# Optimization experiments

Hardware: AMD Instinct MI355X
Metric: run time of the kernel (lower is better)

Reference implementation:

```python
import jax, jax.numpy as jnp
import numpy as np

NUM_CODES = 512
CODE_DIM = 64
COMMITMENT_COST = 0.1
DECAY = 0.9
EPS = 1e-5


def setup_inputs() -> dict:
    key = jax.random.key(0)
    k1, k2, k3 = jax.random.split(key, 3)
    B, L, D, K = 32, 4096, CODE_DIM, NUM_CODES
    z_e = jax.random.normal(k1, (B, L, D), dtype=jnp.float32)
    emb = jax.random.uniform(k2, (K, D), dtype=jnp.float32, minval=-1.0 / K, maxval=1.0 / K)
    ema_cluster_size = jnp.ones((K,), dtype=jnp.float32)
    ema_w = emb + 0.01 * jax.random.normal(k3, (K, D), dtype=jnp.float32)
    return {"z_e": z_e, "emb": emb, "ema_cluster_size": ema_cluster_size, "ema_w": ema_w}


def reference(z_e, emb, ema_cluster_size, ema_w):
    B, L, D = z_e.shape
    K = emb.shape[0]
    flat = z_e.reshape(-1, D)                                   # [N, D]
    dists = (jnp.sum(flat * flat, axis=1, keepdims=True)
             - 2.0 * flat @ emb.T
             + jnp.sum(emb * emb, axis=1)[None, :])
    codes = jnp.argmin(dists, axis=1)                           # [N] int
    z_q = emb[codes].reshape(B, L, D)
    # straight-through estimator
    z_q_st = z_e + jax.lax.stop_gradient(z_q - z_e)
    # EMA updates (training, no_grad) via direct scatter-reduce instead of one-hot matmul
    cluster_size = jax.ops.segment_sum(jnp.ones_like(codes, dtype=z_e.dtype), codes, num_segments=K)
    new_ecs = ema_cluster_size * DECAY + cluster_size * (1.0 - DECAY)
    dw = jax.ops.segment_sum(flat, codes, num_segments=K)       # [K, D]
    new_ema_w = ema_w * DECAY + dw * (1.0 - DECAY)
    n = jnp.sum(new_ecs)
    cs_smoothed = (new_ecs + EPS) / (n + K * EPS) * n
    new_emb = new_ema_w / (cs_smoothed[:, None] + EPS)
    # commitment loss (z_q detached)
    commit = jnp.mean((z_e - jax.lax.stop_gradient(z_q)) ** 2)
    loss_vq = COMMITMENT_COST * commit
    return (z_q_st, loss_vq, codes.reshape(B, L), new_ecs, new_ema_w, new_emb)
```

## Files before the change

### kernel.cpp

```cpp
#include <hip/hip_runtime.h>
#include <math.h>

#define NROWS 131072
#define DIM 64
#define NCODE 512
#define FLAG_CAP 32768
#define THR 6e-5f

#define OUT_ZQ    0
#define OUT_LOSS  8388608
#define OUT_CODES 8388609
#define OUT_ECS   8519681
#define OUT_EMAW  8520193
#define OUT_EMB   8552961

#define WS_LOSS    0
#define WS_N       8
#define WS_FLAGC   12
#define WS_COUNTS  16
#define WS_OFFSETS 2064
#define WS_CURSOR  4112
#define WS_CSUM    6160
#define WS_EHI     8208
#define WS_ELO     73744
#define WS_CODESI  139280
#define WS_DW4     139280
#define WS_BUCKET  663568
#define WS_FLAGR   663568
#define WS_BYTES   1187856
#define WS_ZERO_BYTES 2064

#define DECAY_C ((float)0.9)
#define OMD_C   ((float)(1.0 - 0.9))
#define EPS_C   ((float)1e-5)

typedef float f32x4 __attribute__((ext_vector_type(4)));
typedef short short8v __attribute__((ext_vector_type(8)));

__device__ __forceinline__ unsigned short bf16_rne_bits(float f) {
    unsigned int u = __float_as_uint(f);
    unsigned int r = u + 0x7fffu + ((u >> 16) & 1u);
    return (unsigned short)(r >> 16);
}

__device__ __forceinline__ float np_pairwise64_sq(const float* v) {
    float r[8];
#pragma unroll
    for (int j = 0; j < 8; ++j) r[j] = __fmul_rn(v[j], v[j]);
#pragma unroll
    for (int b = 1; b < 8; ++b) {
#pragma unroll
        for (int j = 0; j < 8; ++j)
            r[j] = __fadd_rn(r[j], __fmul_rn(v[8 * b + j], v[8 * b + j]));
    }
    return __fadd_rn(__fadd_rn(__fadd_rn(r[0], r[1]), __fadd_rn(r[2], r[3])),
                     __fadd_rn(__fadd_rn(r[4], r[5]), __fadd_rn(r[6], r[7])));
}

__global__ void k_csum(const float* __restrict__ emb, float* __restrict__ csum) {
    int k = blockIdx.x * blockDim.x + threadIdx.x;
    if (k >= NCODE) return;
    float e[DIM];
#pragma unroll
    for (int d = 0; d < DIM; d += 4) {
        float4 v = *reinterpret_cast<const float4*>(emb + (size_t)k * DIM + d);
        e[d] = v.x; e[d + 1] = v.y; e[d + 2] = v.z; e[d + 3] = v.w;
    }
    csum[k] = np_pairwise64_sq(e);
}

__global__ __launch_bounds__(256) void k_split(
        const float* __restrict__ emb, unsigned short* __restrict__ ehi,
        unsigned short* __restrict__ elo) {
    int i = blockIdx.x * 256 + threadIdx.x;
    if (i >= NCODE * DIM) return;
    float v = emb[i];
    unsigned short h = bf16_rne_bits(v);
    float hf = __uint_as_float((unsigned int)h << 16);
    ehi[i] = h;
    elo[i] = bf16_rne_bits(v - hf);
}

#define CVTE(H, L, j, val) { \
    unsigned int ub = __float_as_uint(val); \
    unsigned int rr = ub + 0x7fffu + ((ub >> 16) & 1u); \
    unsigned short hb = (unsigned short)(rr >> 16); \
    float hf2 = __uint_as_float(((unsigned int)hb) << 16); \
    float lof = (val) - hf2; \
    unsigned int ul = __float_as_uint(lof); \
    unsigned int rl = ul + 0x7fffu + ((ul >> 16) & 1u); \
    H[j] = (short)hb; L[j] = (short)(rl >> 16); }

__global__ __launch_bounds__(256, 1) void k_mfma(
        const float* __restrict__ ze, const unsigned short* __restrict__ ehi,
        const unsigned short* __restrict__ elo, const float* __restrict__ csum,
        float* __restrict__ out, int* __restrict__ codes_i,
        int* __restrict__ flagC, int* __restrict__ flagR) {
    __shared__ float cs[NCODE];
    for (int i = threadIdx.x; i < NCODE; i += 256) cs[i] = csum[i];
    __syncthreads();
    int wid = threadIdx.x >> 6;
    int lane = threadIdx.x & 63;
    int r16 = lane & 15;
    int kg = lane >> 4;
    int rowbase = blockIdx.x * 128 + wid * 32;

    short8v ahi[2][2], alo[2][2];
#define LOADA(rt, hf) { \
        const float4* ap = reinterpret_cast<const float4*>( \
            ze + (size_t)(rowbase + (rt) * 16 + r16) * DIM + (hf) * 32 + 8 * kg); \
        float4 u = ap[0], w = ap[1]; \
        CVTE(ahi[rt][hf], alo[rt][hf], 0, u.x) CVTE(ahi[rt][hf], alo[rt][hf], 1, u.y) \
        CVTE(ahi[rt][hf], alo[rt][hf], 2, u.z) CVTE(ahi[rt][hf], alo[rt][hf], 3, u.w) \
        CVTE(ahi[rt][hf], alo[rt][hf], 4, w.x) CVTE(ahi[rt][hf], alo[rt][hf], 5, w.y) \
        CVTE(ahi[rt][hf], alo[rt][hf], 6, w.z) CVTE(ahi[rt][hf], alo[rt][hf], 7, w.w) }
    LOADA(0, 0) LOADA(0, 1) LOADA(1, 0) LOADA(1, 1)

    float m1v[2][4], m2v[2][4];
    int i1v[2][4];
#pragma unroll
    for (int rt = 0; rt < 2; ++rt)
#pragma unroll
        for (int j = 0; j < 4; ++j) { m1v[rt][j] = 3.4e38f; m2v[rt][j] = 3.4e38f; i1v[rt][j] = 0; }

#define UPD(C, rt, reg) { \
        float s = __builtin_fmaf(-2.f, C[reg], csv); \
        if (s < m1v[rt][reg]) { m2v[rt][reg] = m1v[rt][reg]; m1v[rt][reg] = s; i1v[rt][reg] = codeIdx; } \
        else if (s < m2v[rt][reg]) { m2v[rt][reg] = s; } }

    for (int t = 0; t < 32; ++t) {
        const short8v* bh = reinterpret_cast<const short8v*>(
            ehi + (size_t)(t * 16 + r16) * DIM + 8 * kg);
        const short8v* bl = reinterpret_cast<const short8v*>(
            elo + (size_t)(t * 16 + r16) * DIM + 8 * kg);
        short8v bh0 = bh[0], bh1 = bh[4];
        short8v bl0 = bl[0], bl1 = bl[4];
        f32x4 c0 = {0.f, 0.f, 0.f, 0.f};
        f32x4 c1 = {0.f, 0.f, 0.f, 0.f};
        c0 = __builtin_amdgcn_mfma_f32_16x16x32_bf16(ahi[0][0], bh0, c0, 0, 0, 0);
        c0 = __builtin_amdgcn_mfma_f32_16x16x32_bf16(ahi[0][1], bh1, c0, 0, 0, 0);
        c0 = __builtin_amdgcn_mfma_f32_16x16x32_bf16(alo[0][0], bh0, c0, 0, 0, 0);
        c0 = __builtin_amdgcn_mfma_f32_16x16x32_bf16(alo[0][1], bh1, c0, 0, 0, 0);
        c0 = __builtin_amdgcn_mfma_f32_16x16x32_bf16(ahi[0][0], bl0, c0, 0, 0, 0);
        c0 = __builtin_amdgcn_mfma_f32_16x16x32_bf16(ahi[0][1], bl1, c0, 0, 0, 0);
        c1 = __builtin_amdgcn_mfma_f32_16x16x32_bf16(ahi[1][0], bh0, c1, 0, 0, 0);
        c1 = __builtin_amdgcn_mfma_f32_16x16x32_bf16(ahi[1][1], bh1, c1, 0, 0, 0);
        c1 = __builtin_amdgcn_mfma_f32_16x16x32_bf16(alo[1][0], bh0, c1, 0, 0, 0);
        c1 = __builtin_amdgcn_mfma_f32_16x16x32_bf16(alo[1][1], bh1, c1, 0, 0, 0);
        c1 = __builtin_amdgcn_mfma_f32_16x16x32_bf16(ahi[1][0], bl0, c1, 0, 0, 0);
        c1 = __builtin_amdgcn_mfma_f32_16x16x32_bf16(ahi[1][1], bl1, c1, 0, 0, 0);
        float csv = cs[t * 16 + r16];
        int codeIdx = t * 16 + r16;
        UPD(c0, 0, 0) UPD(c0, 0, 1) UPD(c0, 0, 2) UPD(c0, 0, 3)
        UPD(c1, 1, 0) UPD(c1, 1, 1) UPD(c1, 1, 2) UPD(c1, 1, 3)
    }

#define RED(rt, reg, mask) { \
        float om1 = __shfl_xor(m1v[rt][reg], mask); \
        int   oi  = __shfl_xor(i1v[rt][reg], mask); \
        float om2 = __shfl_xor(m2v[rt][reg], mask); \
        if (om1 < m1v[rt][reg]) { \
            m2v[rt][reg] = fminf(m1v[rt][reg], om2); m1v[rt][reg] = om1; i1v[rt][reg] = oi; \
        } else if (om1 > m1v[rt][reg]) { \
            m2v[rt][reg] = fminf(m2v[rt][reg], om1); \
        } else { \
            if (oi < i1v[rt][reg]) i1v[rt][reg] = oi; \
            m2v[rt][reg] = m1v[rt][reg]; } }
#define RED4(rt, reg) RED(rt, reg, 1) RED(rt, reg, 2) RED(rt, reg, 4) RED(rt, reg, 8)
    RED4(0, 0) RED4(0, 1) RED4(0, 2) RED4(0, 3)
    RED4(1, 0) RED4(1, 1) RED4(1, 2) RED4(1, 3)

    if (r16 == 0) {
        int g = lane >> 4;
#define WOUT(rt, reg) { \
        int row = rowbase + (rt) * 16 + 4 * g + (reg); \
        out[OUT_CODES + row] = (float)i1v[rt][reg]; \
        codes_i[row] = i1v[rt][reg]; \
        if (m2v[rt][reg] - m1v[rt][reg] < THR) { \
            int pos = atomicAdd(flagC, 1); \
            if (pos < FLAG_CAP) flagR[pos] = row; } }
        WOUT(0, 0) WOUT(0, 1) WOUT(0, 2) WOUT(0, 3)
        WOUT(1, 0) WOUT(1, 1) WOUT(1, 2) WOUT(1, 3)
    }
}

__global__ __launch_bounds__(64) void k_rescue(
        const float* __restrict__ ze, const float* __restrict__ emb,
        const float* __restrict__ csum, float* __restrict__ out,
        int* __restrict__ codes_i, const int* __restrict__ flagC,
        const int* __restrict__ flagR) {
    __shared__ float x2s[DIM];
    int nf = *flagC;
    if (nf > FLAG_CAP) nf = FLAG_CAP;
    int lane = threadIdx.x;
    for (int i = blockIdx.x; i < nf; i += gridDim.x) {
        int row = flagR[i];
        __syncthreads();
        float v = ze[(size_t)row * DIM + lane];
        x2s[lane] = __fadd_rn(v, v);
        __syncthreads();
        float r[8];
#pragma unroll
        for (int j = 0; j < 8; ++j) r[j] = __fmul_rn(x2s[j], x2s[j]);
#pragma unroll
        for (int b = 1; b < 8; ++b) {
#pragma unroll
            for (int j = 0; j < 8; ++j)
                r[j] = __fadd_rn(r[j], __fmul_rn(x2s[8 * b + j], x2s[8 * b + j]));
        }
        float A = __fmul_rn(0.25f,
            __fadd_rn(__fadd_rn(__fadd_rn(r[0], r[1]), __fadd_rn(r[2], r[3])),
                      __fadd_rn(__fadd_rn(r[4], r[5]), __fadd_rn(r[6], r[7]))));
        float m1 = 3.4e38f;
        int i1 = 0x7fffffff;
#pragma unroll
        for (int kk = 0; kk < 8; ++kk) {
            int k = lane * 8 + kk;
            const float* e = emb + (size_t)k * DIM;
            float a = 0.f;
#pragma unroll
            for (int d = 0; d < DIM; ++d) a = __builtin_fmaf(x2s[d], e[d], a);
            float t = __fadd_rn(__fsub_rn(A, a), csum[k]);
            if (t < m1) { m1 = t; i1 = k; }
        }
        for (int off = 32; off; off >>= 1) {
            float ov = __shfl_xor(m1, off);
            int oi = __shfl_xor(i1, off);
            if (ov < m1 || (ov == m1 && oi < i1)) { m1 = ov; i1 = oi; }
        }
        if (lane == 0) {
            out[OUT_CODES + row] = (float)i1;
            codes_i[row] = i1;
        }
    }
}

__global__ __launch_bounds__(256) void k_apply(
        const float* __restrict__ ze, const float* __restrict__ emb,
        const int* __restrict__ codes_i, float* __restrict__ out,
        int* __restrict__ counts, double* __restrict__ lossAcc) {
    __shared__ int h[NCODE];
    __shared__ double ls[4];
    int t = threadIdx.x;
    for (int i = t; i < NCODE; i += 256) h[i] = 0;
    __syncthreads();
    int row = blockIdx.x * 256 + t;
    int code = codes_i[row];
    atomicAdd(&h[code], 1);
    const float* x = ze + (size_t)row * DIM;
    const float* e = emb + (size_t)code * DIM;
    float* zq = out + OUT_ZQ + (size_t)row * DIM;
    double lsum = 0.0;
#pragma unroll
    for (int d = 0; d < DIM; d += 4) {
        float4 xv = *reinterpret_cast<const float4*>(x + d);
        float4 ev = *reinterpret_cast<const float4*>(e + d);
        float ta = __fsub_rn(ev.x, xv.x);
        float tb = __fsub_rn(ev.y, xv.y);
        float tc = __fsub_rn(ev.z, xv.z);
        float td = __fsub_rn(ev.w, xv.w);
        float4 o;
        o.x = __fadd_rn(xv.x, ta);
        o.y = __fadd_rn(xv.y, tb);
        o.z = __fadd_rn(xv.z, tc);
        o.w = __fadd_rn(xv.w, td);
        *reinterpret_cast<float4*>(zq + d) = o;
        lsum += (double)ta * ta + (double)tb * tb + (double)tc * tc + (double)td * td;
    }
    for (int off = 32; off; off >>= 1) lsum += __shfl_down(lsum, off);
    int wid = t >> 6;
    if ((t & 63) == 0) ls[wid] = lsum;
    __syncthreads();
    if (t == 0) atomicAdd(lossAcc, (ls[0] + ls[1]) + (ls[2] + ls[3]));
    for (int k = t; k < NCODE; k += 256) {
        int cc = h[k];
        if (cc) atomicAdd(&counts[k], cc);
    }
}

__global__ __launch_bounds__(512) void k_scan(
        const int* __restrict__ counts, int* __restrict__ offsets, int* __restrict__ cursor,
        const float* __restrict__ ecs_in, float* __restrict__ out, float* __restrict__ n_out) {
    __shared__ int sa[NCODE], sb[NCODE];
    __shared__ float red[NCODE];
    int k = threadIdx.x;
    int c = counts[k];
    sa[k] = c;
    float v = __fadd_rn(__fmul_rn(ecs_in[k], DECAY_C), __fmul_rn((float)c, OMD_C));
    out[OUT_ECS + k] = v;
    red[k] = v;
    __syncthreads();
    int* src = sa;
    int* dst = sb;
    for (int off = 1; off < NCODE; off <<= 1) {
        dst[k] = (k >= off) ? src[k - off] + src[k] : src[k];
        __syncthreads();
        int* tp = src; src = dst; dst = tp;
    }
    offsets[k] = src[k] - c;
    cursor[k]  = src[k] - c;
    for (int s = NCODE / 2; s > 0; s >>= 1) {
        if (k < s) red[k] += red[k + s];
        __syncthreads();
    }
    if (k == 0) n_out[0] = red[0];
}

__global__ __launch_bounds__(256) void k_scatter(
        const int* __restrict__ codes_i, int* __restrict__ cursor, int* __restrict__ bucket) {
    int row = blockIdx.x * 256 + threadIdx.x;
    int c = codes_i[row];
    int pos = atomicAdd(&cursor[c], 1);
    bucket[pos] = row;
}

__global__ __launch_bounds__(256) void k_dw(
        const float* __restrict__ ze, const int* __restrict__ bucket,
        const int* __restrict__ offsets, const int* __restrict__ counts,
        float* __restrict__ dw4) {
    __shared__ float p[4][DIM];
    int k = blockIdx.x >> 2;
    int q = blockIdx.x & 3;
    int w = threadIdx.x >> 6;
    int d = threadIdx.x & 63;
    int s = offsets[k];
    int n = counts[k];
    float acc0 = 0.f, acc1 = 0.f;
    int i = q + 4 * w;
    for (; i + 16 < n; i += 32) {
        int ra = bucket[s + i];
        int rb = bucket[s + i + 16];
        acc0 += ze[(size_t)ra * DIM + d];
        acc1 += ze[(size_t)rb * DIM + d];
    }
    if (i < n) acc0 += ze[(size_t)bucket[s + i] * DIM + d];
    p[w][d] = acc0 + acc1;
    __syncthreads();
    if (w == 0) dw4[((size_t)q * NCODE + k) * DIM + d] = (p[0][d] + p[1][d]) + (p[2][d] + p[3][d]);
}

__global__ __launch_bounds__(256) void k_final(
        const float* __restrict__ ema_w, const float* __restrict__ dw4,
        const float* __restrict__ n_ptr, const double* __restrict__ lossAcc,
        float* __restrict__ out) {
    int i = blockIdx.x * blockDim.x + threadIdx.x;
    if (i >= NCODE * DIM) return;
    int k = i >> 6;
    float dsum = __fadd_rn(__fadd_rn(dw4[i], dw4[i + NCODE * DIM]),
                           __fadd_rn(dw4[i + 2 * NCODE * DIM], dw4[i + 3 * NCODE * DIM]));
    float w = __fadd_rn(__fmul_rn(ema_w[i], DECAY_C), __fmul_rn(dsum, OMD_C));
    out[OUT_EMAW + i] = w;
    float n = n_ptr[0];
    float necs = out[OUT_ECS + k];
    float cs = (necs + EPS_C) / (n + (float)NCODE * EPS_C) * n;
    out[OUT_EMB + i] = w / (cs + EPS_C);
    if (i == 0) out[OUT_LOSS] = (float)(0.1 * (lossAcc[0] / (double)((size_t)NROWS * DIM)));
}

extern "C" void kernel_launch(void* const* d_in, const int* in_sizes, int n_in,
                              void* d_out, int out_size, void* d_ws, size_t ws_size,
                              hipStream_t stream) {
    const float* ze   = (const float*)d_in[0];
    const float* emb  = (const float*)d_in[1];
    const float* ecs  = (const float*)d_in[2];
    const float* emaw = (const float*)d_in[3];
    float* out = (float*)d_out;
    char* ws = (char*)d_ws;
    double* lossAcc = (double*)(ws + WS_LOSS);
    float*  n_out   = (float*)(ws + WS_N);
    int*    flagC   = (int*)(ws + WS_FLAGC);
    int*    counts  = (int*)(ws + WS_COUNTS);
    int*    offsets = (int*)(ws + WS_OFFSETS);
    int*    cursor  = (int*)(ws + WS_CURSOR);
    float*  csum    = (float*)(ws + WS_CSUM);
    unsigned short* ehi = (unsigned short*)(ws + WS_EHI);
    unsigned short* elo = (unsigned short*)(ws + WS_ELO);
    int*    codes_i = (int*)(ws + WS_CODESI);
    float*  dw4     = (float*)(ws + WS_DW4);
    int*    bucket  = (int*)(ws + WS_BUCKET);
    int*    flagR   = (int*)(ws + WS_FLAGR);

    hipMemsetAsync(d_ws, 0, WS_ZERO_BYTES, stream);
    hipLaunchKernelGGL(k_csum, dim3(2), dim3(256), 0, stream, emb, csum);
    hipLaunchKernelGGL(k_split, dim3(NCODE * DIM / 256), dim3(256), 0, stream, emb, ehi, elo);
    hipLaunchKernelGGL(k_mfma, dim3(NROWS / 128), dim3(256), 0, stream,
                       ze, ehi, elo, csum, out, codes_i, flagC, flagR);
    hipLaunchKernelGGL(k_rescue, dim3(1024), dim3(64), 0, stream,
                       ze, emb, csum, out, codes_i, flagC, flagR);
    hipLaunchKernelGGL(k_apply, dim3(NROWS / 256), dim3(256), 0, stream,
                       ze, emb, codes_i, out, counts, lossAcc);
    hipLaunchKernelGGL(k_scan, dim3(1), dim3(512), 0, stream,
                       counts, offsets, cursor, ecs, out, n_out);
    hipLaunchKernelGGL(k_scatter, dim3(NROWS / 256), dim3(256), 0, stream,
                       codes_i, cursor, bucket);
    hipLaunchKernelGGL(k_dw, dim3(NCODE * 4), dim3(256), 0, stream,
                       ze, bucket, offsets, counts, dw4);
    hipLaunchKernelGGL(k_final, dim3(NCODE * DIM / 256), dim3(256), 0, stream,
                       emaw, dw4, n_out, lossAcc, out);
}
```

Before: 225.9 us.

## Fuse z_q gather, loss and histogram into MFMA kernel; patch rescued rows incrementally

The separate apply kernel is removed. The MFMA argmin kernel now writes z_q, accumulates the commitment loss and builds the per-code histogram itself, so z_e is not reread in an extra pass and one launch goes away. The rescue kernel only touches rows whose code actually changes, fixing counts, z_q and the loss by delta. Each block now covers 64 rows instead of 128 (one 16-row tile per wave), and the occupancy hint in launch_bounds is dropped. The cost is less reuse of the B tiles per wave, and the double-precision loss sum is now accumulated in a different order.

```diff
diff --git a/kernel.cpp b/kernel.cpp
--- a/kernel.cpp
+++ b/kernel.cpp
@@ -91,42 +91,45 @@
     unsigned int rl = ul + 0x7fffu + ((ul >> 16) & 1u); \
     H[j] = (short)hb; L[j] = (short)(rl >> 16); }
 
-__global__ __launch_bounds__(256, 1) void k_mfma(
-        const float* __restrict__ ze, const unsigned short* __restrict__ ehi,
-        const unsigned short* __restrict__ elo, const float* __restrict__ csum,
-        float* __restrict__ out, int* __restrict__ codes_i,
-        int* __restrict__ flagC, int* __restrict__ flagR) {
+__global__ __launch_bounds__(256) void k_mfma(
+        const float* __restrict__ ze, const float* __restrict__ emb,
+        const unsigned short* __restrict__ ehi, const unsigned short* __restrict__ elo,
+        const float* __restrict__ csum, float* __restrict__ out,
+        int* __restrict__ codes_i, int* __restrict__ counts,
+        double* __restrict__ lossAcc, int* __restrict__ flagC, int* __restrict__ flagR) {
     __shared__ float cs[NCODE];
-    for (int i = threadIdx.x; i < NCODE; i += 256) cs[i] = csum[i];
-    __syncthreads();
-    int wid = threadIdx.x >> 6;
-    int lane = threadIdx.x & 63;
+    __shared__ int h[NCODE];
+    __shared__ int code_s[64];
+    __shared__ double ls[4];
+    int tid = threadIdx.x;
+    for (int i = tid; i < NCODE; i += 256) { cs[i] = csum[i]; h[i] = 0; }
+    __syncthreads();
+    int wid = tid >> 6;
+    int lane = tid & 63;
     int r16 = lane & 15;
     int kg = lane >> 4;
-    int rowbase = blockIdx.x * 128 + wid * 32;
-
-    short8v ahi[2][2], alo[2][2];
-#define LOADA(rt, hf) { \
+    int blockRow = blockIdx.x * 64;
+    int waveRow = blockRow + wid * 16;
+
+    short8v ahi[2], alo[2];
+#define LOADA(hf) { \
         const float4* ap = reinterpret_cast<const float4*>( \
-            ze + (size_t)(rowbase + (rt) * 16 + r16) * DIM + (hf) * 32 + 8 * kg); \
+            ze + (size_t)(waveRow + r16) * DIM + (hf) * 32 + 8 * kg); \
         float4 u = ap[0], w = ap[1]; \
-        CVTE(ahi[rt][hf], alo[rt][hf], 0, u.x) CVTE(ahi[rt][hf], alo[rt][hf], 1, u.y) \
-        CVTE(ahi[rt][hf], alo[rt][hf], 2, u.z) CVTE(ahi[rt][hf], alo[rt][hf], 3, u.w) \
-        CVTE(ahi[rt][hf], alo[rt][hf], 4, w.x) CVTE(ahi[rt][hf], alo[rt][hf], 5, w.y) \
-        CVTE(ahi[rt][hf], alo[rt][hf], 6, w.z) CVTE(ahi[rt][hf], alo[rt][hf], 7, w.w) }
-    LOADA(0, 0) LOADA(0, 1) LOADA(1, 0) LOADA(1, 1)
-
-    float m1v[2][4], m2v[2][4];
-    int i1v[2][4];
-#pragma unroll
-    for (int rt = 0; rt < 2; ++rt)
-#pragma unroll
-        for (int j = 0; j < 4; ++j) { m1v[rt][j] = 3.4e38f; m2v[rt][j] = 3.4e38f; i1v[rt][j] = 0; }
-
-#define UPD(C, rt, reg) { \
-        float s = __builtin_fmaf(-2.f, C[reg], csv); \
-        if (s < m1v[rt][reg]) { m2v[rt][reg] = m1v[rt][reg]; m1v[rt][reg] = s; i1v[rt][reg] = codeIdx; } \
-        else if (s < m2v[rt][reg]) { m2v[rt][reg] = s; } }
+        CVTE(ahi[hf], alo[hf], 0, u.x) CVTE(ahi[hf], alo[hf], 1, u.y) \
+        CVTE(ahi[hf], alo[hf], 2, u.z) CVTE(ahi[hf], alo[hf], 3, u.w) \
+        CVTE(ahi[hf], alo[hf], 4, w.x) CVTE(ahi[hf], alo[hf], 5, w.y) \
+        CVTE(ahi[hf], alo[hf], 6, w.z) CVTE(ahi[hf], alo[hf], 7, w.w) }
+    LOADA(0) LOADA(1)
+
+    float m1v[4] = {3.4e38f, 3.4e38f, 3.4e38f, 3.4e38f};
+    float m2v[4] = {3.4e38f, 3.4e38f, 3.4e38f, 3.4e38f};
+    int i1v[4] = {0, 0, 0, 0};
+
+#define UPD(reg) { \
+        float s = __builtin_fmaf(-2.f, c[reg], csv); \
+        if (s < m1v[reg]) { m2v[reg] = m1v[reg]; m1v[reg] = s; i1v[reg] = codeIdx; } \
+        else if (s < m2v[reg]) { m2v[reg] = s; } }
 
     for (int t = 0; t < 32; ++t) {
         const short8v* bh = reinterpret_cast<const short8v*>(
@@ -135,59 +138,73 @@
             elo + (size_t)(t * 16 + r16) * DIM + 8 * kg);
         short8v bh0 = bh[0], bh1 = bh[4];
         short8v bl0 = bl[0], bl1 = bl[4];
-        f32x4 c0 = {0.f, 0.f, 0.f, 0.f};
-        f32x4 c1 = {0.f, 0.f, 0.f, 0.f};
-        c0 = __builtin_amdgcn_mfma_f32_16x16x32_bf16(ahi[0][0], bh0, c0, 0, 0, 0);
-        c0 = __builtin_amdgcn_mfma_f32_16x16x32_bf16(ahi[0][1], bh1, c0, 0, 0, 0);
-        c0 = __builtin_amdgcn_mfma_f32_16x16x32_bf16(alo[0][0], bh0, c0, 0, 0, 0);
-        c0 = __builtin_amdgcn_mfma_f32_16x16x32_bf16(alo[0][1], bh1, c0, 0, 0, 0);
-        c0 = __builtin_amdgcn_mfma_f32_16x16x32_bf16(ahi[0][0], bl0, c0, 0, 0, 0);
-        c0 = __builtin_amdgcn_mfma_f32_16x16x32_bf16(ahi[0][1], bl1, c0, 0, 0, 0);
-        c1 = __builtin_amdgcn_mfma_f32_16x16x32_bf16(ahi[1][0], bh0, c1, 0, 0, 0);
-        c1 = __builtin_amdgcn_mfma_f32_16x16x32_bf16(ahi[1][1], bh1, c1, 0, 0, 0);
-        c1 = __builtin_amdgcn_mfma_f32_16x16x32_bf16(alo[1][0], bh0, c1, 0, 0, 0);
-        c1 = __builtin_amdgcn_mfma_f32_16x16x32_bf16(alo[1][1], bh1, c1, 0, 0, 0);
-        c1 = __builtin_amdgcn_mfma_f32_16x16x32_bf16(ahi[1][0], bl0, c1, 0, 0, 0);
-        c1 = __builtin_amdgcn_mfma_f32_16x16x32_bf16(ahi[1][1], bl1, c1, 0, 0, 0);
+        f32x4 c = {0.f, 0.f, 0.f, 0.f};
+        c = __builtin_amdgcn_mfma_f32_16x16x32_bf16(ahi[0], bh0, c, 0, 0, 0);
+        c = __builtin_amdgcn_mfma_f32_16x16x32_bf16(ahi[1], bh1, c, 0, 0, 0);
+        c = __builtin_amdgcn_mfma_f32_16x16x32_bf16(alo[0], bh0, c, 0, 0, 0);
+        c = __builtin_amdgcn_mfma_f32_16x16x32_bf16(alo[1], bh1, c, 0, 0, 0);
+        c = __builtin_amdgcn_mfma_f32_16x16x32_bf16(ahi[0], bl0, c, 0, 0, 0);
+        c = __builtin_amdgcn_mfma_f32_16x16x32_bf16(ahi[1], bl1, c, 0, 0, 0);
         float csv = cs[t * 16 + r16];
         int codeIdx = t * 16 + r16;
-        UPD(c0, 0, 0) UPD(c0, 0, 1) UPD(c0, 0, 2) UPD(c0, 0, 3)
-        UPD(c1, 1, 0) UPD(c1, 1, 1) UPD(c1, 1, 2) UPD(c1, 1, 3)
-    }
-
-#define RED(rt, reg, mask) { \
-        float om1 = __shfl_xor(m1v[rt][reg], mask); \
-        int   oi  = __shfl_xor(i1v[rt][reg], mask); \
-        float om2 = __shfl_xor(m2v[rt][reg], mask); \
-        if (om1 < m1v[rt][reg]) { \
-            m2v[rt][reg] = fminf(m1v[rt][reg], om2); m1v[rt][reg] = om1; i1v[rt][reg] = oi; \
-        } else if (om1 > m1v[rt][reg]) { \
-            m2v[rt][reg] = fminf(m2v[rt][reg], om1); \
+        UPD(0) UPD(1) UPD(2) UPD(3)
+    }
+
+#define RED(reg, mask) { \
+        float om1 = __shfl_xor(m1v[reg], mask); \
+        int   oi  = __shfl_xor(i1v[reg], mask); \
+        float om2 = __shfl_xor(m2v[reg], mask); \
+        if (om1 < m1v[reg]) { \
+            m2v[reg] = fminf(m1v[reg], om2); m1v[reg] = om1; i1v[reg] = oi; \
+        } else if (om1 > m1v[reg]) { \
+            m2v[reg] = fminf(m2v[reg], om1); \
         } else { \
-            if (oi < i1v[rt][reg]) i1v[rt][reg] = oi; \
-            m2v[rt][reg] = m1v[rt][reg]; } }
-#define RED4(rt, reg) RED(rt, reg, 1) RED(rt, reg, 2) RED(rt, reg, 4) RED(rt, reg, 8)
-    RED4(0, 0) RED4(0, 1) RED4(0, 2) RED4(0, 3)
-    RED4(1, 0) RED4(1, 1) RED4(1, 2) RED4(1, 3)
+            if (oi < i1v[reg]) i1v[reg] = oi; \
+            m2v[reg] = m1v[reg]; } }
+#define RED4(reg) RED(reg, 1) RED(reg, 2) RED(reg, 4) RED(reg, 8)
+    RED4(0) RED4(1) RED4(2) RED4(3)
 
     if (r16 == 0) {
-        int g = lane >> 4;
-#define WOUT(rt, reg) { \
-        int row = rowbase + (rt) * 16 + 4 * g + (reg); \
-        out[OUT_CODES + row] = (float)i1v[rt][reg]; \
-        codes_i[row] = i1v[rt][reg]; \
-        if (m2v[rt][reg] - m1v[rt][reg] < THR) { \
+#define WOUT(reg) { \
+        int lrow = wid * 16 + 4 * kg + (reg); \
+        int row = blockRow + lrow; \
+        code_s[lrow] = i1v[reg]; \
+        out[OUT_CODES + row] = (float)i1v[reg]; \
+        codes_i[row] = i1v[reg]; \
+        atomicAdd(&h[i1v[reg]], 1); \
+        if (m2v[reg] - m1v[reg] < THR) { \
             int pos = atomicAdd(flagC, 1); \
             if (pos < FLAG_CAP) flagR[pos] = row; } }
-        WOUT(0, 0) WOUT(0, 1) WOUT(0, 2) WOUT(0, 3)
-        WOUT(1, 0) WOUT(1, 1) WOUT(1, 2) WOUT(1, 3)
+        WOUT(0) WOUT(1) WOUT(2) WOUT(3)
+    }
+    __syncthreads();
+
+    double lpart = 0.0;
+#pragma unroll 4
+    for (int r = 0; r < 16; ++r) {
+        int code = code_s[wid * 16 + r];
+        int row = waveRow + r;
+        float x = ze[(size_t)row * DIM + lane];
+        float e = emb[(size_t)code * DIM + lane];
+        float tdiff = __fsub_rn(e, x);
+        out[OUT_ZQ + (size_t)row * DIM + lane] = __fadd_rn(x, tdiff);
+        lpart += (double)tdiff * tdiff;
+    }
+    for (int off = 32; off; off >>= 1) lpart += __shfl_down(lpart, off);
+    if (lane == 0) ls[wid] = lpart;
+    __syncthreads();
+    if (tid == 0) atomicAdd(lossAcc, (ls[0] + ls[1]) + (ls[2] + ls[3]));
+    for (int k = tid; k < NCODE; k += 256) {
+        int cc = h[k];
+        if (cc) atomicAdd(&counts[k], cc);
     }
 }
 
 __global__ __launch_bounds__(64) void k_rescue(
         const float* __restrict__ ze, const float* __restrict__ emb,
         const float* __restrict__ csum, float* __restrict__ out,
-        int* __restrict__ codes_i, const int* __restrict__ flagC,
+        int* __restrict__ codes_i, int* __restrict__ counts,
+        double* __restrict__ lossAcc, const int* __restrict__ flagC,
         const int* __restrict__ flagR) {
     __shared__ float x2s[DIM];
     int nf = *flagC;
@@ -228,53 +245,24 @@
             int oi = __shfl_xor(i1, off);
             if (ov < m1 || (ov == m1 && oi < i1)) { m1 = ov; i1 = oi; }
         }
-        if (lane == 0) {
-            out[OUT_CODES + row] = (float)i1;
-            codes_i[row] = i1;
+        int oldc = codes_i[row];
+        if (i1 != oldc) {
+            if (lane == 0) {
+                codes_i[row] = i1;
+                out[OUT_CODES + row] = (float)i1;
+                atomicSub(&counts[oldc], 1);
+                atomicAdd(&counts[i1], 1);
+            }
+            float x = __fmul_rn(0.5f, x2s[lane]);
+            float en = emb[(size_t)i1 * DIM + lane];
+            float eo = emb[(size_t)oldc * DIM + lane];
+            float tn = __fsub_rn(en, x);
+            float to = __fsub_rn(eo, x);
+            out[OUT_ZQ + (size_t)row * DIM + lane] = __fadd_rn(x, tn);
+            double dl = (double)tn * tn - (double)to * to;
+            for (int off = 32; off; off >>= 1) dl += __shfl_down(dl, off);
+            if (lane == 0) atomicAdd(lossAcc, dl);
         }
-    }
-}
-
-__global__ __launch_bounds__(256) void k_apply(
-        const float* __restrict__ ze, const float* __restrict__ emb,
-        const int* __restrict__ codes_i, float* __restrict__ out,
-        int* __restrict__ counts, double* __restrict__ lossAcc) {
-    __shared__ int h[NCODE];
-    __shared__ double ls[4];
-    int t = threadIdx.x;
-    for (int i = t; i < NCODE; i += 256) h[i] = 0;
-    __syncthreads();
-    int row = blockIdx.x * 256 + t;
-    int code = codes_i[row];
-    atomicAdd(&h[code], 1);
-    const float* x = ze + (size_t)row * DIM;
-    const float* e = emb + (size_t)code * DIM;
-    float* zq = out + OUT_ZQ + (size_t)row * DIM;
-    double lsum = 0.0;
-#pragma unroll
-    for (int d = 0; d < DIM; d += 4) {
-        float4 xv = *reinterpret_cast<const float4*>(x + d);
-        float4 ev = *reinterpret_cast<const float4*>(e + d);
-        float ta = __fsub_rn(ev.x, xv.x);
-        float tb = __fsub_rn(ev.y, xv.y);
-        float tc = __fsub_rn(ev.z, xv.z);
-        float td = __fsub_rn(ev.w, xv.w);
-        float4 o;
-        o.x = __fadd_rn(xv.x, ta);
-        o.y = __fadd_rn(xv.y, tb);
-        o.z = __fadd_rn(xv.z, tc);
-        o.w = __fadd_rn(xv.w, td);
-        *reinterpret_cast<float4*>(zq + d) = o;
-        lsum += (double)ta * ta + (double)tb * tb + (double)tc * tc + (double)td * td;
-    }
-    for (int off = 32; off; off >>= 1) lsum += __shfl_down(lsum, off);
-    int wid = t >> 6;
-    if ((t & 63) == 0) ls[wid] = lsum;
-    __syncthreads();
-    if (t == 0) atomicAdd(lossAcc, (ls[0] + ls[1]) + (ls[2] + ls[3]));
-    for (int k = t; k < NCODE; k += 256) {
-        int cc = h[k];
-        if (cc) atomicAdd(&counts[k], cc);
     }
 }
 
@@ -383,12 +371,10 @@
     hipMemsetAsync(d_ws, 0, WS_ZERO_BYTES, stream);
     hipLaunchKernelGGL(k_csum, dim3(2), dim3(256), 0, stream, emb, csum);
     hipLaunchKernelGGL(k_split, dim3(NCODE * DIM / 256), dim3(256), 0, stream, emb, ehi, elo);
-    hipLaunchKernelGGL(k_mfma, dim3(NROWS / 128), dim3(256), 0, stream,
-                       ze, ehi, elo, csum, out, codes_i, flagC, flagR);
+    hipLaunchKernelGGL(k_mfma, dim3(NROWS / 64), dim3(256), 0, stream,
+                       ze, emb, ehi, elo, csum, out, codes_i, counts, lossAcc, flagC, flagR);
     hipLaunchKernelGGL(k_rescue, dim3(1024), dim3(64), 0, stream,
-                       ze, emb, csum, out, codes_i, flagC, flagR);
-    hipLaunchKernelGGL(k_apply, dim3(NROWS / 256), dim3(256), 0, stream,
-                       ze, emb, codes_i, out, counts, lossAcc);
+                       ze, emb, csum, out, codes_i, counts, lossAcc, flagC, flagR);
     hipLaunchKernelGGL(k_scan, dim3(1), dim3(512), 0, stream,
                        counts, offsets, cursor, ecs, out, n_out);
     hipLaunchKernelGGL(k_scatter, dim3(NROWS / 256), dim3(256), 0, stream,
```

Result: slower. 310.5 us (+37.5%).

## Fuse z_q gather, loss, and code histogram into the MFMA argmin kernel

Applied to the files above, without the earlier changes.

Removes the separate apply kernel by computing the code histogram, the z_q straight-through output and the commitment loss inside the MFMA kernel, right after the argmin. The rescue kernel now applies corrections as deltas: it adjusts counts, rewrites z_q and adds the loss difference when a flagged row's code changes. This saves a full extra read of z_e and a kernel launch. In exchange the MFMA kernel carries more work, and the rescue path gains atomics.

```diff
diff --git a/kernel.cpp b/kernel.cpp
--- a/kernel.cpp
+++ b/kernel.cpp
@@ -92,15 +92,20 @@
     H[j] = (short)hb; L[j] = (short)(rl >> 16); }
 
 __global__ __launch_bounds__(256, 1) void k_mfma(
-        const float* __restrict__ ze, const unsigned short* __restrict__ ehi,
-        const unsigned short* __restrict__ elo, const float* __restrict__ csum,
-        float* __restrict__ out, int* __restrict__ codes_i,
-        int* __restrict__ flagC, int* __restrict__ flagR) {
+        const float* __restrict__ ze, const float* __restrict__ emb,
+        const unsigned short* __restrict__ ehi, const unsigned short* __restrict__ elo,
+        const float* __restrict__ csum, float* __restrict__ out,
+        int* __restrict__ codes_i, int* __restrict__ counts,
+        double* __restrict__ lossAcc, int* __restrict__ flagC, int* __restrict__ flagR) {
     __shared__ float cs[NCODE];
-    for (int i = threadIdx.x; i < NCODE; i += 256) cs[i] = csum[i];
-    __syncthreads();
-    int wid = threadIdx.x >> 6;
-    int lane = threadIdx.x & 63;
+    __shared__ int h[NCODE];
+    __shared__ int code_s[128];
+    __shared__ double ls[4];
+    int tid = threadIdx.x;
+    for (int i = tid; i < NCODE; i += 256) { cs[i] = csum[i]; h[i] = 0; }
+    __syncthreads();
+    int wid = tid >> 6;
+    int lane = tid & 63;
     int r16 = lane & 15;
     int kg = lane >> 4;
     int rowbase = blockIdx.x * 128 + wid * 32;
@@ -171,23 +176,47 @@
     RED4(1, 0) RED4(1, 1) RED4(1, 2) RED4(1, 3)
 
     if (r16 == 0) {
-        int g = lane >> 4;
 #define WOUT(rt, reg) { \
-        int row = rowbase + (rt) * 16 + 4 * g + (reg); \
+        int lrow = wid * 32 + (rt) * 16 + 4 * kg + (reg); \
+        int row = blockIdx.x * 128 + lrow; \
+        code_s[lrow] = i1v[rt][reg]; \
         out[OUT_CODES + row] = (float)i1v[rt][reg]; \
         codes_i[row] = i1v[rt][reg]; \
+        atomicAdd(&h[i1v[rt][reg]], 1); \
         if (m2v[rt][reg] - m1v[rt][reg] < THR) { \
             int pos = atomicAdd(flagC, 1); \
             if (pos < FLAG_CAP) flagR[pos] = row; } }
         WOUT(0, 0) WOUT(0, 1) WOUT(0, 2) WOUT(0, 3)
         WOUT(1, 0) WOUT(1, 1) WOUT(1, 2) WOUT(1, 3)
     }
+    __syncthreads();
+
+    double lpart = 0.0;
+#pragma unroll 4
+    for (int r = 0; r < 32; ++r) {
+        int code = code_s[wid * 32 + r];
+        int row = rowbase + r;
+        float x = ze[(size_t)row * DIM + lane];
+        float e = emb[(size_t)code * DIM + lane];
+        float tdiff = __fsub_rn(e, x);
+        out[OUT_ZQ + (size_t)row * DIM + lane] = __fadd_rn(x, tdiff);
+        lpart += (double)tdiff * tdiff;
+    }
+    for (int off = 32; off; off >>= 1) lpart += __shfl_down(lpart, off);
+    if (lane == 0) ls[wid] = lpart;
+    __syncthreads();
+    if (tid == 0) atomicAdd(lossAcc, (ls[0] + ls[1]) + (ls[2] + ls[3]));
+    for (int k = tid; k < NCODE; k += 256) {
+        int cc = h[k];
+        if (cc) atomicAdd(&counts[k], cc);
+    }
 }
 
 __global__ __launch_bounds__(64) void k_rescue(
         const float* __restrict__ ze, const float* __restrict__ emb,
         const float* __restrict__ csum, float* __restrict__ out,
-        int* __restrict__ codes_i, const int* __restrict__ flagC,
+        int* __restrict__ codes_i, int* __restrict__ counts,
+        double* __restrict__ lossAcc, const int* __restrict__ flagC,
         const int* __restrict__ flagR) {
     __shared__ float x2s[DIM];
     int nf = *flagC;
@@ -228,53 +257,24 @@
             int oi = __shfl_xor(i1, off);
             if (ov < m1 || (ov == m1 && oi < i1)) { m1 = ov; i1 = oi; }
         }
-        if (lane == 0) {
-            out[OUT_CODES + row] = (float)i1;
-            codes_i[row] = i1;
+        int oldc = codes_i[row];
+        if (i1 != oldc) {
+            if (lane == 0) {
+                codes_i[row] = i1;
+                out[OUT_CODES + row] = (float)i1;
+                atomicSub(&counts[oldc], 1);
+                atomicAdd(&counts[i1], 1);
+            }
+            float x = __fmul_rn(0.5f, x2s[lane]);
+            float en = emb[(size_t)i1 * DIM + lane];
+            float eo = emb[(size_t)oldc * DIM + lane];
+            float tn = __fsub_rn(en, x);
+            float to = __fsub_rn(eo, x);
+            out[OUT_ZQ + (size_t)row * DIM + lane] = __fadd_rn(x, tn);
+            double dl = (double)tn * tn - (double)to * to;
+            for (int off = 32; off; off >>= 1) dl += __shfl_down(dl, off);
+            if (lane == 0) atomicAdd(lossAcc, dl);
         }
-    }
-}
-
-__global__ __launch_bounds__(256) void k_apply(
-        const float* __restrict__ ze, const float* __restrict__ emb,
-        const int* __restrict__ codes_i, float* __restrict__ out,
-        int* __restrict__ counts, double* __restrict__ lossAcc) {
-    __shared__ int h[NCODE];
-    __shared__ double ls[4];
-    int t = threadIdx.x;
-    for (int i = t; i < NCODE; i += 256) h[i] = 0;
-    __syncthreads();
-    int row = blockIdx.x * 256 + t;
-    int code = codes_i[row];
-    atomicAdd(&h[code], 1);
-    const float* x = ze + (size_t)row * DIM;
-    const float* e = emb + (size_t)code * DIM;
-    float* zq = out + OUT_ZQ + (size_t)row * DIM;
-    double lsum = 0.0;
-#pragma unroll
-    for (int d = 0; d < DIM; d += 4) {
-        float4 xv = *reinterpret_cast<const float4*>(x + d);
-        float4 ev = *reinterpret_cast<const float4*>(e + d);
-        float ta = __fsub_rn(ev.x, xv.x);
-        float tb = __fsub_rn(ev.y, xv.y);
-        float tc = __fsub_rn(ev.z, xv.z);
-        float td = __fsub_rn(ev.w, xv.w);
-        float4 o;
-        o.x = __fadd_rn(xv.x, ta);
-        o.y = __fadd_rn(xv.y, tb);
-        o.z = __fadd_rn(xv.z, tc);
-        o.w = __fadd_rn(xv.w, td);
-        *reinterpret_cast<float4*>(zq + d) = o;
-        lsum += (double)ta * ta + (double)tb * tb + (double)tc * tc + (double)td * td;
-    }
-    for (int off = 32; off; off >>= 1) lsum += __shfl_down(lsum, off);
-    int wid = t >> 6;
-    if ((t & 63) == 0) ls[wid] = lsum;
-    __syncthreads();
-    if (t == 0) atomicAdd(lossAcc, (ls[0] + ls[1]) + (ls[2] + ls[3]));
-    for (int k = t; k < NCODE; k += 256) {
-        int cc = h[k];
-        if (cc) atomicAdd(&counts[k], cc);
     }
 }
 
@@ -384,11 +384,9 @@
     hipLaunchKernelGGL(k_csum, dim3(2), dim3(256), 0, stream, emb, csum);
     hipLaunchKernelGGL(k_split, dim3(NCODE * DIM / 256), dim3(256), 0, stream, emb, ehi, elo);
     hipLaunchKernelGGL(k_mfma, dim3(NROWS / 128), dim3(256), 0, stream,
-                       ze, ehi, elo, csum, out, codes_i, flagC, flagR);
+                       ze, emb, ehi, elo, csum, out, codes_i, counts, lossAcc, flagC, flagR);
     hipLaunchKernelGGL(k_rescue, dim3(1024), dim3(64), 0, stream,
-                       ze, emb, csum, out, codes_i, flagC, flagR);
-    hipLaunchKernelGGL(k_apply, dim3(NROWS / 256), dim3(256), 0, stream,
-                       ze, emb, codes_i, out, counts, lossAcc);
+                       ze, emb, csum, out, codes_i, counts, lossAcc, flagC, flagR);
     hipLaunchKernelGGL(k_scan, dim3(1), dim3(512), 0, stream,
                        counts, offsets, cursor, ecs, out, n_out);
     hipLaunchKernelGGL(k_scatter, dim3(NROWS / 256), dim3(256), 0, stream,
```

After: 226.5 us. No clear change (+0.2%).
